# Kernel tuning notes

Hardware: AMD Instinct MI355X
Metric: run time of the kernel (lower is better)

## Reference

```python
import jax, jax.numpy as jnp
import numpy as np
import math

E, K = 8, 4
IN, OUT = 768, 768
B, S = 16, 512

def _nearest_factors(n):
    r = int(math.sqrt(n))
    while n % r != 0:
        r -= 1
    r = max(r, 1)
    return r, n // r

D1, D2 = _nearest_factors(IN)      # 24, 32
DO1, DO2 = _nearest_factors(OUT)   # 24, 32

def _cv_squared(v):
    v = v.astype(jnp.float32)
    return jnp.var(v, ddof=1) / (jnp.mean(v) ** 2 + 1e-10)

def setup_inputs() -> dict:
    key = jax.random.key(0)
    ks = jax.random.split(key, 8)
    eye = lambda d: jnp.broadcast_to(jnp.eye(d, dtype=jnp.float32), (E, d, d))
    return {
        "x": jax.random.normal(ks[0], (B, S, IN), jnp.float32),
        "w_gate": 0.02 * jax.random.normal(ks[1], (IN, E), jnp.float32),
        "weight": 0.02 * jax.random.normal(ks[2], (E, OUT, IN), jnp.float32),
        "res_weight": 0.02 * jax.random.normal(ks[3], (OUT, IN), jnp.float32),
        "curve1_in": eye(D1) + 0.01 * jax.random.normal(ks[4], (E, D1, D1), jnp.float32),
        "curve2_in": eye(D2) + 0.01 * jax.random.normal(ks[5], (E, D2, D2), jnp.float32),
        "curve1_out": eye(DO1) + 0.01 * jax.random.normal(ks[6], (E, DO1, DO1), jnp.float32),
        "curve2_out": eye(DO2) + 0.01 * jax.random.normal(ks[7], (E, DO2, DO2), jnp.float32),
    }

def reference(x, w_gate, weight, res_weight, curve1_in, curve2_in, curve1_out, curve2_out):
    b = x.shape[0]
    # ---- noisy_top_k_gating (eval mode: clean logits, no noise) ----
    xm = x.mean(-2)                         # [B, IN]
    logits = xm @ w_gate                    # [B, E]
    top_vals, top_idx = jax.lax.top_k(logits, min(K + 1, E))
    tk_vals = top_vals[:, :K]
    tk_idx = top_idx[:, :K]
    tk_gates = jax.nn.softmax(tk_vals, axis=1)
    gates = jnp.zeros_like(logits).at[jnp.arange(b)[:, None], tk_idx].set(tk_gates)
    load = (gates > 0).sum(0)               # eval: gates_to_load
    importance = gates.sum(0)
    loss = 0.01 * (_cv_squared(importance) + _cv_squared(load))
    # ---- curve-factor expert weight composition (k*2 >= n_experts branch) ----
    rtw = (weight - res_weight).reshape(E, DO1, DO2, D1, D2)
    rtw = jnp.einsum('bij,bjklm->biklm', curve1_out, rtw)
    rtw = jnp.einsum('bik,bjklm->bjilm', curve2_out, rtw)
    rtw = jnp.einsum('bil,bjklm->bjkim', curve1_in, rtw)
    rtw = jnp.einsum('bim,bjklm->bjkli', curve2_in, rtw)
    rtw = rtw.reshape(E, OUT, IN)
    # dropout p=0.1 is identity in eval mode
    expert_weights = res_weight + 0.9 * jnp.sum(rtw[None] * gates[:, :, None, None], axis=1)  # [B, OUT, IN]
    y = jnp.einsum('bsj,bkj->bsk', x, expert_weights)  # [B, S, OUT]
    return y, loss
```

## Files before the change

### kernel.cpp

```cpp
#include <hip/hip_runtime.h>
#include <hip/hip_bf16.h>
#include <hip/hip_cooperative_groups.h>

namespace cg = cooperative_groups;

typedef unsigned short u16;
typedef __attribute__((ext_vector_type(8))) short bf16x8;
typedef __attribute__((ext_vector_type(4))) float f32x4;

#define NE 8
#define NTOPK 4
#define NIN 768
#define NOUT 768
#define NB 16
#define NS 512
#define YSZ (NB * NS * NOUT)
#define EWN (NOUT * NIN)
#define NBLK 768

#define OFF_PART  0u
#define OFF_GATES 3145728u
#define OFF_XBF   3146240u
#define OFF_WD    15729152u
#define OFF_T1T   25166336u
#define OFF_RTW   34603520u
#define OFF_EW    44040704u

#define PRE_BAR(N) asm volatile("s_waitcnt vmcnt(" #N ")\n\ts_barrier" ::: "memory")
#define POST_BAR() asm volatile("s_waitcnt lgkmcnt(0)\n\ts_barrier" ::: "memory")

__device__ __forceinline__ u16 f2bf(float f) {
  union { float f; unsigned u; } v; v.f = f;
  unsigned r = v.u + 0x7fffu + ((v.u >> 16) & 1u);
  return (u16)(r >> 16);
}
__device__ __forceinline__ float bf2f(u16 h) {
  union { unsigned u; float f; } v; v.u = ((unsigned)h) << 16;
  return v.f;
}
__device__ __forceinline__ unsigned cvt2(float a, float b) {
  unsigned r;
  asm("v_cvt_pk_bf16_f32 %0, %1, %2" : "=v"(r) : "v"(a), "v"(b));
  return r;
}
__device__ __forceinline__ void gload16(const void* g, void* l) {
  __builtin_amdgcn_global_load_lds(
      (const __attribute__((address_space(1))) unsigned int*)g,
      (__attribute__((address_space(3))) unsigned int*)l, 16, 0, 0);
}
__device__ __forceinline__ void storeC(float* p, float v) { *p = v; }
__device__ __forceinline__ void storeC(u16* p, float v) { *p = f2bf(v); }

__device__ __forceinline__ void body_xmwd(int u, const float* __restrict__ x,
                                          float* __restrict__ part, u16* __restrict__ xbf,
                                          const float* __restrict__ w,
                                          const float* __restrict__ res,
                                          u16* __restrict__ Wd) {
  if (u < 1024) {
    int t = threadIdx.x;
    if (t < 192) {
      int b = u >> 6;
      int sc = u & 63;
      int c = t * 4;
      float a0 = 0.f, a1 = 0.f, a2 = 0.f, a3 = 0.f;
      int s0 = sc * 8;
#pragma unroll
      for (int r = 0; r < 8; ++r) {
        size_t ro = ((size_t)(b * NS + s0 + r)) * NIN;
        float4 v = *(const float4*)(x + ro + c);
        a0 += v.x; a1 += v.y; a2 += v.z; a3 += v.w;
        ushort4 o;
        o.x = f2bf(v.x); o.y = f2bf(v.y); o.z = f2bf(v.z); o.w = f2bf(v.w);
        *(ushort4*)(xbf + ro + c) = o;
      }
      float4 pv; pv.x = a0; pv.y = a1; pv.z = a2; pv.w = a3;
      *(float4*)(part + (size_t)(b * 64 + sc) * NIN + c) = pv;
    }
  } else {
    int b2 = u - 1024;
    int e = b2 / 288;
    int blk = b2 % 288;
    size_t base = (size_t)blk * 2048 + threadIdx.x * 8;
    float4 wa = *(const float4*)(w + (size_t)e * EWN + base);
    float4 wb = *(const float4*)(w + (size_t)e * EWN + base + 4);
    float4 ra = *(const float4*)(res + base);
    float4 rb = *(const float4*)(res + base + 4);
    bf16x8 o;
    o[0] = (short)f2bf(wa.x - ra.x); o[1] = (short)f2bf(wa.y - ra.y);
    o[2] = (short)f2bf(wa.z - ra.z); o[3] = (short)f2bf(wa.w - ra.w);
    o[4] = (short)f2bf(wb.x - rb.x); o[5] = (short)f2bf(wb.y - rb.y);
    o[6] = (short)f2bf(wb.z - rb.z); o[7] = (short)f2bf(wb.w - rb.w);
    *(bf16x8*)(Wd + (size_t)e * EWN + base) = o;
  }
}

__device__ __forceinline__ void body_logits(int b, float* red,
                                            const float* __restrict__ part,
                                            const float* __restrict__ w_gate,
                                            float* __restrict__ gates_out) {
  int tid = threadIdx.x;
  float p[NE] = {0.f, 0.f, 0.f, 0.f, 0.f, 0.f, 0.f, 0.f};
  for (int i = tid; i < NIN; i += 256) {
    float s = 0.f;
#pragma unroll
    for (int sc = 0; sc < 64; ++sc) s += part[(size_t)(b * 64 + sc) * NIN + i];
    float xmv = s * (1.0f / (float)NS);
#pragma unroll
    for (int e = 0; e < NE; ++e) p[e] += xmv * w_gate[i * NE + e];
  }
#pragma unroll
  for (int e = 0; e < NE; ++e) {
    float v = p[e];
    for (int off = 32; off; off >>= 1) v += __shfl_down(v, off);
    if ((tid & 63) == 0) red[(tid >> 6) * NE + e] = v;
  }
  __syncthreads();
  if (tid == 0) {
    float v[NE]; bool used[NE];
    for (int e = 0; e < NE; ++e) {
      v[e] = red[e] + red[NE + e] + red[2 * NE + e] + red[3 * NE + e];
      used[e] = false;
    }
    int idxs[NTOPK]; float vals[NTOPK];
    for (int t = 0; t < NTOPK; ++t) {
      int best = 0; float bv = -3.4e38f;
      for (int e = 0; e < NE; ++e)
        if (!used[e] && v[e] > bv) { bv = v[e]; best = e; }
      used[best] = true; idxs[t] = best; vals[t] = bv;
    }
    float m = vals[0];
    float ex[NTOPK]; float se = 0.f;
    for (int t = 0; t < NTOPK; ++t) { ex[t] = expf(vals[t] - m); se += ex[t]; }
    float g[NE];
    for (int e = 0; e < NE; ++e) g[e] = 0.f;
    for (int t = 0; t < NTOPK; ++t) g[idxs[t]] = ex[t] / se;
    for (int e = 0; e < NE; ++e) gates_out[b * NE + e] = g[e];
  }
}

__device__ __forceinline__ void body_kron(int bid, u16* lb,
                                          const float* __restrict__ c1,
                                          const float* __restrict__ c2,
                                          const u16* __restrict__ B,
                                          u16* __restrict__ C) {
  const int tid = threadIdx.x;
  const int lane = tid & 63;
  const int w = tid >> 6;
  const int wr = w >> 1, wc = w & 1;
  const int fr = lane & 15;
  const int kq = lane >> 4;
  const int swz = (bid & 7) * 72 + (bid >> 3);
  const int mb = swz % 12;
  const int nb = (swz / 12) % 6;
  const int e = swz / 72;
  const int m0 = mb * 64, n0 = nb * 128;
  const u16* Bb = B + (size_t)e * EWN;
  const float* c1b = c1 + e * 24 * 24;
  const float* c2b = c2 + e * 32 * 32;
  const int r1a = (m0 >> 5) + wr;
  float c2r[2][8];
  {
    const float* p0 = c2b + fr * 32 + kq * 8;
    const float* p1 = c2b + (16 + fr) * 32 + kq * 8;
#pragma unroll
    for (int j = 0; j < 8; ++j) { c2r[0][j] = p0[j]; c2r[1][j] = p1[j]; }
  }
  const int ob1 = (w * 2) * 1024 + lane * 16;
  const int ob2 = ob1 + 1024;
  const int rowB1 = ob1 >> 6, colB1 = ob1 & 63;
  const int rowB2 = ob2 >> 6, colB2 = ob2 & 63;

  auto STAGE = [&](int t) {
    int s = t & 3;
    int k0 = t * 32;
    gload16((const char*)Bb + ((size_t)(n0 + rowB1) * NIN + k0) * 2 + colB1,
            (char*)(lb + s * 4096) + ob1);
    gload16((const char*)Bb + ((size_t)(n0 + rowB2) * NIN + k0) * 2 + colB2,
            (char*)(lb + s * 4096) + ob2);
  };
  f32x4 acc[2][4] = {};
  auto COMPUTE = [&](int t) {
    int s = t & 3;
    const float ca = c1b[r1a * 24 + t];
    bf16x8 aF[2], bF[4];
#pragma unroll
    for (int m = 0; m < 2; ++m) {
      const float* cr = c2r[m];
      union { unsigned u[4]; bf16x8 v; } pk;
      pk.u[0] = cvt2(ca * cr[0], ca * cr[1]);
      pk.u[1] = cvt2(ca * cr[2], ca * cr[3]);
      pk.u[2] = cvt2(ca * cr[4], ca * cr[5]);
      pk.u[3] = cvt2(ca * cr[6], ca * cr[7]);
      aF[m] = pk.v;
    }
#pragma unroll
    for (int n = 0; n < 4; ++n)
      bF[n] = *(const bf16x8*)(lb + (size_t)s * 4096 + (wc * 64 + n * 16 + fr) * 32 + kq * 8);
#pragma unroll
    for (int m = 0; m < 2; ++m)
#pragma unroll
      for (int n = 0; n < 4; ++n)
        acc[m][n] = __builtin_amdgcn_mfma_f32_16x16x32_bf16(aF[m], bF[n], acc[m][n], 0, 0, 0);
  };

  STAGE(0); STAGE(1); STAGE(2); STAGE(3);
  for (int i = 0; i < 10; ++i) {
    PRE_BAR(4);
    COMPUTE(2 * i); COMPUTE(2 * i + 1);
    POST_BAR();
    STAGE(2 * i + 4); STAGE(2 * i + 5);
  }
  PRE_BAR(4);  COMPUTE(20); COMPUTE(21);  POST_BAR();
  PRE_BAR(0);  COMPUTE(22); COMPUTE(23);

  u16* Cb = C + (size_t)e * EWN;
#pragma unroll
  for (int m = 0; m < 2; ++m) {
    int rb = m0 + wr * 32 + m * 16 + kq * 4;
#pragma unroll
    for (int n = 0; n < 4; ++n) {
      int col = n0 + wc * 64 + n * 16 + fr;
#pragma unroll
      for (int r = 0; r < 4; ++r)
        storeC(Cb + (size_t)(rb + r) * NIN + col, acc[m][n][r]);
    }
  }
}

__device__ __forceinline__ void body_combine(int bid, float* gsh,
                                             const u16* __restrict__ rtwb,
                                             const float* __restrict__ res,
                                             const float* __restrict__ g,
                                             u16* __restrict__ ew,
                                             float* __restrict__ loss_out) {
  int tid = threadIdx.x;
  if (tid < NB * NE) gsh[tid] = 0.9f * g[tid];
  __syncthreads();
  if (bid == 0 && tid == 0) {
    float imp[NE], ld[NE];
    for (int e = 0; e < NE; ++e) {
      float si = 0.f, sl = 0.f;
      for (int b = 0; b < NB; ++b) {
        float gg = g[b * NE + e];
        si += gg; sl += (gg > 0.f) ? 1.f : 0.f;
      }
      imp[e] = si; ld[e] = sl;
    }
    float loss = 0.f;
    for (int which = 0; which < 2; ++which) {
      const float* a = which ? ld : imp;
      float mean = 0.f;
      for (int e = 0; e < NE; ++e) mean += a[e];
      mean *= (1.0f / NE);
      float var = 0.f;
      for (int e = 0; e < NE; ++e) { float d = a[e] - mean; var += d * d; }
      var *= (1.0f / (NE - 1));
      loss += var / (mean * mean + 1e-10f);
    }
    loss_out[0] = 0.01f * loss;
  }
  size_t base = ((size_t)bid * 256 + tid) * 8;
  float rv[NE][8];
#pragma unroll
  for (int e = 0; e < NE; ++e) {
    bf16x8 v = *(const bf16x8*)(rtwb + (size_t)e * EWN + base);
#pragma unroll
    for (int j = 0; j < 8; ++j) rv[e][j] = bf2f((u16)v[j]);
  }
  float r8[8];
  {
    float4 ra = *(const float4*)(res + base);
    float4 rb = *(const float4*)(res + base + 4);
    r8[0] = ra.x; r8[1] = ra.y; r8[2] = ra.z; r8[3] = ra.w;
    r8[4] = rb.x; r8[5] = rb.y; r8[6] = rb.z; r8[7] = rb.w;
  }
  for (int b = 0; b < NB; ++b) {
    float a[8];
#pragma unroll
    for (int j = 0; j < 8; ++j) a[j] = r8[j];
#pragma unroll
    for (int e = 0; e < NE; ++e) {
      float gg = gsh[b * NE + e];
#pragma unroll
      for (int j = 0; j < 8; ++j) a[j] += gg * rv[e][j];
    }
    bf16x8 o;
#pragma unroll
    for (int j = 0; j < 8; ++j) o[j] = (short)f2bf(a[j]);
    *(bf16x8*)(ew + (size_t)b * EWN + base) = o;
  }
}

__global__ __launch_bounds__(256, 3) void mega(const float* __restrict__ x,
                                               const float* __restrict__ w_gate,
                                               const float* __restrict__ weight,
                                               const float* __restrict__ res_w,
                                               const float* __restrict__ c1i,
                                               const float* __restrict__ c2i,
                                               const float* __restrict__ c1o,
                                               const float* __restrict__ c2o,
                                               float* part, float* gates,
                                               u16* xbf, u16* Wd, u16* T1t, u16* rtwb,
                                               u16* ew, float* lossp) {
  __shared__ __attribute__((aligned(128))) u16 lB0[4 * 128 * 32];
  __shared__ float red[NB * NE];
  cg::grid_group grid = cg::this_grid();
  const int bid = blockIdx.x;

  for (int u = bid; u < 3328; u += NBLK)
    body_xmwd(u, x, part, xbf, weight, res_w, Wd);
  grid.sync();

  if (bid < 576)       body_kron(bid, lB0, c1i, c2i, Wd, T1t);
  else if (bid < 592)  body_logits(bid - 576, red, part, w_gate, gates);
  grid.sync();

  if (bid < 576)       body_kron(bid, lB0, c1o, c2o, T1t, rtwb);
  grid.sync();

  if (bid < 288)       body_combine(bid, red, rtwb, res_w, gates, ew, lossp);
}

__global__ __launch_bounds__(256, 2) void k_main(const u16* __restrict__ A,
                                                 const u16* __restrict__ Bw,
                                                 float* __restrict__ C) {
  __shared__ __attribute__((aligned(128))) u16 la[4 * 128 * 32];
  __shared__ __attribute__((aligned(128))) u16 lb[4 * 128 * 32];
  const int tid = threadIdx.x;
  const int lane = tid & 63;
  const int w = tid >> 6;
  const int wr = w >> 1, wc = w & 1;
  const int fr = lane & 15;
  const int kq = lane >> 4;
  const int swz = (blockIdx.x & 7) * 48 + (blockIdx.x >> 3);
  const int mb = swz % 4;
  const int nb = (swz / 4) % 6;
  const int b = swz / 24;
  const int m0 = mb * 128, n0 = nb * 128;
  const u16* Ab = A + (size_t)b * NS * NIN;
  const u16* Bb = Bw + (size_t)b * EWN;
  const int ob1 = tid * 16;
  const int ob2 = ob1 + 4096;
  const int row1 = ob1 >> 6, col1 = ob1 & 63;
  const int row2 = ob2 >> 6, col2 = ob2 & 63;

  auto STAGE = [&](int t) {
    int s = t & 3;
    int k0 = t * 32;
    gload16((const char*)Ab + ((size_t)(m0 + row1) * NIN + k0) * 2 + col1,
            (char*)(la + s * 4096) + ob1);
    gload16((const char*)Ab + ((size_t)(m0 + row2) * NIN + k0) * 2 + col2,
            (char*)(la + s * 4096) + ob2);
    gload16((const char*)Bb + ((size_t)(n0 + row1) * NIN + k0) * 2 + col1,
            (char*)(lb + s * 4096) + ob1);
    gload16((const char*)Bb + ((size_t)(n0 + row2) * NIN + k0) * 2 + col2,
            (char*)(lb + s * 4096) + ob2);
  };
  f32x4 acc[4][4] = {};
  auto COMPUTE = [&](int t) {
    int s = t & 3;
    bf16x8 aF[4], bF[4];
#pragma unroll
    for (int m = 0; m < 4; ++m)
      aF[m] = *(const bf16x8*)(la + (size_t)s * 4096 + (wr * 64 + m * 16 + fr) * 32 + kq * 8);
#pragma unroll
    for (int n = 0; n < 4; ++n)
      bF[n] = *(const bf16x8*)(lb + (size_t)s * 4096 + (wc * 64 + n * 16 + fr) * 32 + kq * 8);
#pragma unroll
    for (int m = 0; m < 4; ++m)
#pragma unroll
      for (int n = 0; n < 4; ++n)
        acc[m][n] = __builtin_amdgcn_mfma_f32_16x16x32_bf16(aF[m], bF[n], acc[m][n], 0, 0, 0);
  };

  STAGE(0); STAGE(1); STAGE(2); STAGE(3);
  for (int i = 0; i < 10; ++i) {
    PRE_BAR(8);
    COMPUTE(2 * i); COMPUTE(2 * i + 1);
    POST_BAR();
    STAGE(2 * i + 4); STAGE(2 * i + 5);
  }
  PRE_BAR(8);  COMPUTE(20); COMPUTE(21);  POST_BAR();
  PRE_BAR(0);  COMPUTE(22); COMPUTE(23);

  float* Cb = C + (size_t)b * NS * NOUT;
#pragma unroll
  for (int m = 0; m < 4; ++m) {
    int rb = m0 + wr * 64 + m * 16 + kq * 4;
#pragma unroll
    for (int n = 0; n < 4; ++n) {
      int col = n0 + wc * 64 + n * 16 + fr;
#pragma unroll
      for (int r = 0; r < 4; ++r)
        Cb[(size_t)(rb + r) * NOUT + col] = acc[m][n][r];
    }
  }
}

__global__ __launch_bounds__(256) void k_p0(const float* x, float* part, u16* xbf,
                                            const float* w, const float* res, u16* Wd) {
  body_xmwd(blockIdx.x, x, part, xbf, w, res, Wd);
}
__global__ __launch_bounds__(256) void k_p1(const float* c1, const float* c2,
                                            const u16* B, u16* C,
                                            const float* part, const float* w_gate,
                                            float* gates) {
  __shared__ __attribute__((aligned(128))) u16 lB[4 * 128 * 32];
  __shared__ float red[NB * NE];
  if (blockIdx.x < 576) body_kron(blockIdx.x, lB, c1, c2, B, C);
  else                  body_logits(blockIdx.x - 576, red, part, w_gate, gates);
}
__global__ __launch_bounds__(256) void k_p2(const float* c1, const float* c2,
                                            const u16* B, u16* C) {
  __shared__ __attribute__((aligned(128))) u16 lB[4 * 128 * 32];
  body_kron(blockIdx.x, lB, c1, c2, B, C);
}
__global__ __launch_bounds__(256) void k_p3(const u16* rtwb, const float* res,
                                            const float* g, u16* ew, float* loss) {
  __shared__ float gsh[NB * NE];
  body_combine(blockIdx.x, gsh, rtwb, res, g, ew, loss);
}

extern "C" void kernel_launch(void* const* d_in, const int* in_sizes, int n_in,
                              void* d_out, int out_size, void* d_ws, size_t ws_size,
                              hipStream_t stream) {
  const float* x = (const float*)d_in[0];
  const float* w_gate = (const float*)d_in[1];
  const float* weight = (const float*)d_in[2];
  const float* res_w = (const float*)d_in[3];
  const float* c1i = (const float*)d_in[4];
  const float* c2i = (const float*)d_in[5];
  const float* c1o = (const float*)d_in[6];
  const float* c2o = (const float*)d_in[7];

  char* ws = (char*)d_ws;
  float* part = (float*)(ws + OFF_PART);
  float* gates = (float*)(ws + OFF_GATES);
  u16* xbf = (u16*)(ws + OFF_XBF);
  u16* Wd = (u16*)(ws + OFF_WD);
  u16* T1t = (u16*)(ws + OFF_T1T);
  u16* rtwb = (u16*)(ws + OFF_RTW);
  u16* ew = (u16*)(ws + OFF_EW);

  float* y = (float*)d_out;
  float* loss = y + YSZ;

  int occ = 0;
  bool coop =
      (hipOccupancyMaxActiveBlocksPerMultiprocessor(&occ, mega, 256, 0) == hipSuccess) &&
      occ >= 3;
  if (coop) {
    void* args[] = {(void*)&x, (void*)&w_gate, (void*)&weight, (void*)&res_w,
                    (void*)&c1i, (void*)&c2i, (void*)&c1o, (void*)&c2o,
                    (void*)&part, (void*)&gates, (void*)&xbf, (void*)&Wd,
                    (void*)&T1t, (void*)&rtwb, (void*)&ew, (void*)&loss};
    coop = (hipLaunchCooperativeKernel((const void*)mega, dim3(NBLK), dim3(256),
                                       args, 0, stream) == hipSuccess);
  }
  if (!coop) {
    k_p0<<<dim3(3328), 256, 0, stream>>>(x, part, xbf, weight, res_w, Wd);
    k_p1<<<dim3(592), 256, 0, stream>>>(c1i, c2i, Wd, T1t, part, w_gate, gates);
    k_p2<<<dim3(576), 256, 0, stream>>>(c1o, c2o, T1t, rtwb);
    k_p3<<<dim3(288), 256, 0, stream>>>(rtwb, res_w, gates, ew, loss);
  }
  k_main<<<dim3(384), 256, 0, stream>>>(xbf, ew, y);
}
```

Before: 77.09 us.

## Drop cooperative megakernel for separate launches and use 3-stage GEMM pipeline

Removes the cooperative persistent kernel with grid syncs and always runs the four prep phases as separate kernel launches. The main GEMM moves from a 4-stage LDS ring consuming two k-tiles per barrier to a 3-stage ring consuming one tile per barrier, and drops the min-blocks launch bound. This avoids grid-sync overhead and the forced occupancy of the megakernel, but adds launch gaps, doubles the barrier count in the GEMM loop, and uses a modulo-3 stage index.

New measurement: 79.63 us. 1.03x slower.

```diff
diff --git a/kernel.cpp b/kernel.cpp
--- a/kernel.cpp
+++ b/kernel.cpp
@@ -1,8 +1,5 @@
 #include <hip/hip_runtime.h>
 #include <hip/hip_bf16.h>
-#include <hip/hip_cooperative_groups.h>
-
-namespace cg = cooperative_groups;
 
 typedef unsigned short u16;
 typedef __attribute__((ext_vector_type(8))) short bf16x8;
@@ -16,7 +13,6 @@
 #define NS 512
 #define YSZ (NB * NS * NOUT)
 #define EWN (NOUT * NIN)
-#define NBLK 768
 
 #define OFF_PART  0u
 #define OFF_GATES 3145728u
@@ -51,11 +47,13 @@
 __device__ __forceinline__ void storeC(float* p, float v) { *p = v; }
 __device__ __forceinline__ void storeC(u16* p, float v) { *p = f2bf(v); }
 
-__device__ __forceinline__ void body_xmwd(int u, const float* __restrict__ x,
-                                          float* __restrict__ part, u16* __restrict__ xbf,
-                                          const float* __restrict__ w,
-                                          const float* __restrict__ res,
-                                          u16* __restrict__ Wd) {
+__global__ __launch_bounds__(256) void k_p0(const float* __restrict__ x,
+                                            float* __restrict__ part,
+                                            u16* __restrict__ xbf,
+                                            const float* __restrict__ w,
+                                            const float* __restrict__ res,
+                                            u16* __restrict__ Wd) {
+  int u = blockIdx.x;
   if (u < 1024) {
     int t = threadIdx.x;
     if (t < 192) {
@@ -227,12 +225,28 @@
   }
 }
 
-__device__ __forceinline__ void body_combine(int bid, float* gsh,
-                                             const u16* __restrict__ rtwb,
-                                             const float* __restrict__ res,
-                                             const float* __restrict__ g,
-                                             u16* __restrict__ ew,
-                                             float* __restrict__ loss_out) {
+__global__ __launch_bounds__(256) void k_p1(const float* c1, const float* c2,
+                                            const u16* B, u16* C,
+                                            const float* part, const float* w_gate,
+                                            float* gates) {
+  __shared__ __attribute__((aligned(128))) u16 lB[4 * 128 * 32];
+  __shared__ float red[NB * NE];
+  if (blockIdx.x < 576) body_kron(blockIdx.x, lB, c1, c2, B, C);
+  else                  body_logits(blockIdx.x - 576, red, part, w_gate, gates);
+}
+__global__ __launch_bounds__(256) void k_p2(const float* c1, const float* c2,
+                                            const u16* B, u16* C) {
+  __shared__ __attribute__((aligned(128))) u16 lB[4 * 128 * 32];
+  body_kron(blockIdx.x, lB, c1, c2, B, C);
+}
+
+__global__ __launch_bounds__(256) void k_p3(const u16* __restrict__ rtwb,
+                                            const float* __restrict__ res,
+                                            const float* __restrict__ g,
+                                            u16* __restrict__ ew,
+                                            float* __restrict__ loss_out) {
+  __shared__ float gsh[NB * NE];
+  int bid = blockIdx.x;
   int tid = threadIdx.x;
   if (tid < NB * NE) gsh[tid] = 0.9f * g[tid];
   __syncthreads();
@@ -291,41 +305,11 @@
   }
 }
 
-__global__ __launch_bounds__(256, 3) void mega(const float* __restrict__ x,
-                                               const float* __restrict__ w_gate,
-                                               const float* __restrict__ weight,
-                                               const float* __restrict__ res_w,
-                                               const float* __restrict__ c1i,
-                                               const float* __restrict__ c2i,
-                                               const float* __restrict__ c1o,
-                                               const float* __restrict__ c2o,
-                                               float* part, float* gates,
-                                               u16* xbf, u16* Wd, u16* T1t, u16* rtwb,
-                                               u16* ew, float* lossp) {
-  __shared__ __attribute__((aligned(128))) u16 lB0[4 * 128 * 32];
-  __shared__ float red[NB * NE];
-  cg::grid_group grid = cg::this_grid();
-  const int bid = blockIdx.x;
-
-  for (int u = bid; u < 3328; u += NBLK)
-    body_xmwd(u, x, part, xbf, weight, res_w, Wd);
-  grid.sync();
-
-  if (bid < 576)       body_kron(bid, lB0, c1i, c2i, Wd, T1t);
-  else if (bid < 592)  body_logits(bid - 576, red, part, w_gate, gates);
-  grid.sync();
-
-  if (bid < 576)       body_kron(bid, lB0, c1o, c2o, T1t, rtwb);
-  grid.sync();
-
-  if (bid < 288)       body_combine(bid, red, rtwb, res_w, gates, ew, lossp);
-}
-
-__global__ __launch_bounds__(256, 2) void k_main(const u16* __restrict__ A,
-                                                 const u16* __restrict__ Bw,
-                                                 float* __restrict__ C) {
-  __shared__ __attribute__((aligned(128))) u16 la[4 * 128 * 32];
-  __shared__ __attribute__((aligned(128))) u16 lb[4 * 128 * 32];
+__global__ __launch_bounds__(256) void k_main(const u16* __restrict__ A,
+                                              const u16* __restrict__ Bw,
+                                              float* __restrict__ C) {
+  __shared__ __attribute__((aligned(128))) u16 la[3 * 128 * 32];
+  __shared__ __attribute__((aligned(128))) u16 lb[3 * 128 * 32];
   const int tid = threadIdx.x;
   const int lane = tid & 63;
   const int w = tid >> 6;
@@ -345,7 +329,7 @@
   const int row2 = ob2 >> 6, col2 = ob2 & 63;
 
   auto STAGE = [&](int t) {
-    int s = t & 3;
+    int s = t % 3;
     int k0 = t * 32;
     gload16((const char*)Ab + ((size_t)(m0 + row1) * NIN + k0) * 2 + col1,
             (char*)(la + s * 4096) + ob1);
@@ -358,7 +342,7 @@
   };
   f32x4 acc[4][4] = {};
   auto COMPUTE = [&](int t) {
-    int s = t & 3;
+    int s = t % 3;
     bf16x8 aF[4], bF[4];
 #pragma unroll
     for (int m = 0; m < 4; ++m)
@@ -373,15 +357,16 @@
         acc[m][n] = __builtin_amdgcn_mfma_f32_16x16x32_bf16(aF[m], bF[n], acc[m][n], 0, 0, 0);
   };
 
-  STAGE(0); STAGE(1); STAGE(2); STAGE(3);
-  for (int i = 0; i < 10; ++i) {
+  STAGE(0); STAGE(1); STAGE(2);
+  for (int t = 0; t < 21; ++t) {
     PRE_BAR(8);
-    COMPUTE(2 * i); COMPUTE(2 * i + 1);
+    COMPUTE(t);
     POST_BAR();
-    STAGE(2 * i + 4); STAGE(2 * i + 5);
-  }
-  PRE_BAR(8);  COMPUTE(20); COMPUTE(21);  POST_BAR();
-  PRE_BAR(0);  COMPUTE(22); COMPUTE(23);
+    STAGE(t + 3);
+  }
+  PRE_BAR(8);  COMPUTE(21);  POST_BAR();
+  PRE_BAR(4);  COMPUTE(22);  POST_BAR();
+  PRE_BAR(0);  COMPUTE(23);
 
   float* Cb = C + (size_t)b * NS * NOUT;
 #pragma unroll
@@ -395,30 +380,6 @@
         Cb[(size_t)(rb + r) * NOUT + col] = acc[m][n][r];
     }
   }
-}
-
-__global__ __launch_bounds__(256) void k_p0(const float* x, float* part, u16* xbf,
-                                            const float* w, const float* res, u16* Wd) {
-  body_xmwd(blockIdx.x, x, part, xbf, w, res, Wd);
-}
-__global__ __launch_bounds__(256) void k_p1(const float* c1, const float* c2,
-                                            const u16* B, u16* C,
-                                            const float* part, const float* w_gate,
-                                            float* gates) {
-  __shared__ __attribute__((aligned(128))) u16 lB[4 * 128 * 32];
-  __shared__ float red[NB * NE];
-  if (blockIdx.x < 576) body_kron(blockIdx.x, lB, c1, c2, B, C);
-  else                  body_logits(blockIdx.x - 576, red, part, w_gate, gates);
-}
-__global__ __launch_bounds__(256) void k_p2(const float* c1, const float* c2,
-                                            const u16* B, u16* C) {
-  __shared__ __attribute__((aligned(128))) u16 lB[4 * 128 * 32];
-  body_kron(blockIdx.x, lB, c1, c2, B, C);
-}
-__global__ __launch_bounds__(256) void k_p3(const u16* rtwb, const float* res,
-                                            const float* g, u16* ew, float* loss) {
-  __shared__ float gsh[NB * NE];
-  body_combine(blockIdx.x, gsh, rtwb, res, g, ew, loss);
 }
 
 extern "C" void kernel_launch(void* const* d_in, const int* in_sizes, int n_in,
@@ -445,23 +406,9 @@
   float* y = (float*)d_out;
   float* loss = y + YSZ;
 
-  int occ = 0;
-  bool coop =
-      (hipOccupancyMaxActiveBlocksPerMultiprocessor(&occ, mega, 256, 0) == hipSuccess) &&
-      occ >= 3;
-  if (coop) {
-    void* args[] = {(void*)&x, (void*)&w_gate, (void*)&weight, (void*)&res_w,
-                    (void*)&c1i, (void*)&c2i, (void*)&c1o, (void*)&c2o,
-                    (void*)&part, (void*)&gates, (void*)&xbf, (void*)&Wd,
-                    (void*)&T1t, (void*)&rtwb, (void*)&ew, (void*)&loss};
-    coop = (hipLaunchCooperativeKernel((const void*)mega, dim3(NBLK), dim3(256),
-                                       args, 0, stream) == hipSuccess);
-  }
-  if (!coop) {
-    k_p0<<<dim3(3328), 256, 0, stream>>>(x, part, xbf, weight, res_w, Wd);
-    k_p1<<<dim3(592), 256, 0, stream>>>(c1i, c2i, Wd, T1t, part, w_gate, gates);
-    k_p2<<<dim3(576), 256, 0, stream>>>(c1o, c2o, T1t, rtwb);
-    k_p3<<<dim3(288), 256, 0, stream>>>(rtwb, res_w, gates, ew, loss);
-  }
+  k_p0<<<dim3(3328), 256, 0, stream>>>(x, part, xbf, weight, res_w, Wd);
+  k_p1<<<dim3(592), 256, 0, stream>>>(c1i, c2i, Wd, T1t, part, w_gate, gates);
+  k_p2<<<dim3(576), 256, 0, stream>>>(c1o, c2o, T1t, rtwb);
+  k_p3<<<dim3(288), 256, 0, stream>>>(rtwb, res_w, gates, ew, loss);
   k_main<<<dim3(384), 256, 0, stream>>>(xbf, ew, y);
 }
```
